# Performance work log

Hardware: AMD Instinct MI355X
Metric: run time of the kernel (lower is better)

Reference implementation:

```python
import jax, jax.numpy as jnp
import numpy as np

HIDDEN = 32
FEATURES = 16
LABELS = 4
T = 8
N = 40000
E = 640000
D_IN = FEATURES + LABELS + HIDDEN + 1  # GATv2Conv input dim = 53


def setup_inputs() -> dict:
    key = jax.random.key(0)
    ks = jax.random.split(key, 16)
    x = jax.random.normal(ks[0], (T, N, FEATURES), dtype=jnp.float32)
    mask = (jax.random.uniform(ks[1], (N,)) < 0.7).astype(jnp.float32)
    labels = jax.random.normal(ks[2], (N, LABELS), dtype=jnp.float32)
    edge_index = jax.random.randint(ks[3], (2, E), 0, N, dtype=jnp.int32)
    edge_weight = jax.random.uniform(ks[4], (E,), dtype=jnp.float32)
    s = 1.0 / np.sqrt(D_IN)
    # 4 GATv2Conv layers stacked: 0=reset, 1=update, 2=cell, 3=final
    Wl = jax.random.normal(ks[5], (4, HIDDEN, D_IN), dtype=jnp.float32) * s
    bl = jnp.zeros((4, HIDDEN), dtype=jnp.float32)
    Wr = jax.random.normal(ks[6], (4, HIDDEN, D_IN), dtype=jnp.float32) * s
    br = jnp.zeros((4, HIDDEN), dtype=jnp.float32)
    att = jax.random.normal(ks[7], (4, HIDDEN), dtype=jnp.float32) * (1.0 / np.sqrt(HIDDEN))
    bconv = jnp.zeros((4, HIDDEN), dtype=jnp.float32)
    W1 = jax.random.normal(ks[8], (FEATURES, HIDDEN), dtype=jnp.float32) * (1.0 / np.sqrt(HIDDEN))
    b1 = jnp.zeros((FEATURES,), dtype=jnp.float32)
    W2 = jax.random.normal(ks[9], (FEATURES, 2 * HIDDEN), dtype=jnp.float32) * (1.0 / np.sqrt(2 * HIDDEN))
    b2 = jnp.zeros((FEATURES,), dtype=jnp.float32)
    return {"x": x, "mask": mask, "labels": labels, "edge_index": edge_index,
            "edge_weight": edge_weight, "Wl": Wl, "bl": bl, "Wr": Wr, "br": br,
            "att": att, "bconv": bconv, "W1": W1, "b1": b1, "W2": W2, "b2": b2}


def gatv2(xin, src, dst, Wl, bl, Wr, br, att, bconv):
    # GATv2Conv, heads=1, add_self_loops=False (edge_weight unused: lin_edge is None)
    xl = xin @ Wl.T + bl          # [N, H] source transform (message)
    xr = xin @ Wr.T + br          # [N, H] target transform
    z = jax.nn.leaky_relu(xl[src] + xr[dst], 0.2)  # [E, H]
    e = z @ att                   # [E] attention logits
    m = jax.ops.segment_max(e, dst, num_segments=N)
    a = jnp.exp(e - m[dst])
    den = jax.ops.segment_sum(a, dst, num_segments=N)[dst]
    a = a / jnp.where(den > 0, den, 1.0)
    out = jax.ops.segment_sum(a[:, None] * xl[src], dst, num_segments=N)
    return out + bconv


def reference(x, mask, labels, edge_index, edge_weight, Wl, bl, Wr, br, att, bconv, W1, b1, W2, b2):
    src, dst = edge_index[0], edge_index[1]
    mcol = mask[:, None]                       # [N, 1] float, concatenated as a feature
    mbool = mcol > 0.5                         # [N, 1] bool, used for where()
    masked_input = jnp.where(mbool[None], x, 0.0)  # [T, N, F]
    hidden0 = jnp.ones((N, HIDDEN), dtype=x.dtype)
    x2_0 = masked_input[0]

    def step(carry, xt):
        hidden, x2 = carry
        ft = jnp.concatenate([x2, mcol, labels], axis=1)        # [N, F+1+L]
        inp = jnp.concatenate([ft, hidden], axis=1)             # [N, D_IN]
        reset = jax.nn.sigmoid(gatv2(inp, src, dst, Wl[0], bl[0], Wr[0], br[0], att[0], bconv[0]))
        update = jax.nn.sigmoid(gatv2(inp, src, dst, Wl[1], bl[1], Wr[1], br[1], att[1], bconv[1]))
        cin = jnp.concatenate([ft, reset * hidden], axis=1)
        cell = jnp.tanh(gatv2(cin, src, dst, Wl[2], bl[2], Wr[2], br[2], att[2], bconv[2]))
        hidden = update * hidden + (1.0 - update) * cell        # (dropout inactive: eval mode)
        y1 = hidden @ W1.T + b1
        x1 = jnp.where(mbool, xt, y1)
        ft2 = jnp.concatenate([x1, mcol, hidden, labels], axis=1)  # [N, D_IN]
        s = jax.nn.relu(gatv2(ft2, src, dst, Wl[3], bl[3], Wr[3], br[3], att[3], bconv[3]))
        y2 = jnp.concatenate([s, hidden], axis=1) @ W2.T + b2
        x2_new = jnp.where(mbool, xt, y2)
        return (hidden, x2_new), x2_new

    _, out = jax.lax.scan(step, (hidden0, x2_0), masked_input)
    return out  # [T, N, F]
```

## Files before the change

### kernel.cpp

```cpp
#include <hip/hip_runtime.h>
#include <math.h>

#define NN   40000
#define EE   640000
#define HID  32
#define FEAT 16
#define LAB  4
#define TT   8
#define DIN  53
#define WD   (HID * DIN)


__device__ __forceinline__ unsigned short f2bf(float f) {
    unsigned int u = __float_as_uint(f);
    unsigned int r = u + 0x7fffu + ((u >> 16) & 1u);
    return (unsigned short)(r >> 16);
}
__device__ __forceinline__ float bflo(unsigned int u) { return __uint_as_float(u << 16); }
__device__ __forceinline__ float bfhi(unsigned int u) { return __uint_as_float(u & 0xffff0000u); }
__device__ __forceinline__ void unpack8(uint4 u, float* v) {
    v[0] = bflo(u.x); v[1] = bfhi(u.x);
    v[2] = bflo(u.y); v[3] = bfhi(u.y);
    v[4] = bflo(u.z); v[5] = bfhi(u.z);
    v[6] = bflo(u.w); v[7] = bfhi(u.w);
}


__global__ __launch_bounds__(256) void zero_i32(int* __restrict__ p, int n) {
    int i = blockIdx.x * 256 + threadIdx.x;
    if (i < n) p[i] = 0;
}

__global__ __launch_bounds__(256) void hist_kernel(const int* __restrict__ dst,
                                                   int* __restrict__ deg) {
    int e = blockIdx.x * 256 + threadIdx.x;
    if (e < EE) atomicAdd(&deg[dst[e]], 1);
}

__global__ __launch_bounds__(1024) void scan_kernel(const int* __restrict__ deg,
                                                    int* __restrict__ row_ptr) {
    __shared__ int wsum[16];
    __shared__ int chunk_total;
    int tid = threadIdx.x;
    int lane = tid & 63, wv = tid >> 6;
    int carry = 0;
    if (tid == 0) row_ptr[0] = 0;
    for (int base = 0; base < NN; base += 1024) {
        int i = base + tid;
        int v = (i < NN) ? deg[i] : 0;
        #pragma unroll
        for (int o = 1; o < 64; o <<= 1) {
            int t = __shfl_up(v, o);
            if (lane >= o) v += t;
        }
        if (lane == 63) wsum[wv] = v;
        __syncthreads();
        if (tid < 16) {
            int s = wsum[tid];
            #pragma unroll
            for (int o = 1; o < 16; o <<= 1) {
                int t = __shfl_up(s, o);
                if (tid >= o) s += t;
            }
            wsum[tid] = s;
            if (tid == 15) chunk_total = s;
        }
        __syncthreads();
        int woff = (wv == 0) ? 0 : wsum[wv - 1];
        if (i < NN) row_ptr[i + 1] = carry + woff + v;
        carry += chunk_total;
        __syncthreads();
    }
}

__global__ __launch_bounds__(256) void scatter_kernel(const int* __restrict__ src,
                                                      const int* __restrict__ dst,
                                                      const int* __restrict__ row_ptr,
                                                      int* __restrict__ cursor,
                                                      int* __restrict__ csr_src) {
    int e = blockIdx.x * 256 + threadIdx.x;
    if (e < EE) {
        int d = dst[e];
        int pos = atomicAdd(&cursor[d], 1);
        csr_src[row_ptr[d] + pos] = src[e];
    }
}

__global__ __launch_bounds__(256) void sort_kernel(const int* __restrict__ row_ptr,
                                                   int* __restrict__ csr_src) {
    int n = blockIdx.x * 256 + threadIdx.x;
    if (n < NN) {
        int beg = row_ptr[n], end = row_ptr[n + 1];
        for (int i = beg + 1; i < end; ++i) {
            int key = csr_src[i];
            int j = i - 1;
            while (j >= beg && csr_src[j] > key) {
                csr_src[j + 1] = csr_src[j];
                --j;
            }
            csr_src[j + 1] = key;
        }
    }
}


__global__ __launch_bounds__(256) void init_kernel(const float* __restrict__ x0,
                                                   const float* __restrict__ mask,
                                                   float* __restrict__ hidden,
                                                   float* __restrict__ x2) {
    int i = blockIdx.x * 256 + threadIdx.x;
    if (i < NN * HID) hidden[i] = 1.0f;
    if (i < NN * FEAT) {
        int node = i >> 4;
        x2[i] = (mask[node] > 0.5f) ? x0[i] : 0.0f;
    }
}


__global__ __launch_bounds__(256) void dense01_kernel(const float* __restrict__ feat,
                                                      const float* __restrict__ mask,
                                                      const float* __restrict__ labels,
                                                      const float* __restrict__ hsrc,
                                                      const float* __restrict__ Wl,
                                                      const float* __restrict__ bl,
                                                      const float* __restrict__ Wr,
                                                      const float* __restrict__ br,
                                                      unsigned short* __restrict__ xl01h,
                                                      float* __restrict__ xr01) {
    __shared__ float W_s[4 * WD];
    __shared__ float inp_s[8][DIN];
    for (int idx = threadIdx.x; idx < WD; idx += 256) {
        W_s[idx]          = Wl[idx];
        W_s[WD + idx]     = Wl[WD + idx];
        W_s[2 * WD + idx] = Wr[idx];
        W_s[3 * WD + idx] = Wr[WD + idx];
    }
    int ni = threadIdx.x >> 5, k = threadIdx.x & 31;
    const float* w0 = &W_s[k * DIN];
    const float* w1 = &W_s[WD + k * DIN];
    const float* w2 = &W_s[2 * WD + k * DIN];
    const float* w3 = &W_s[3 * WD + k * DIN];
    float bl0 = bl[k], bl1 = bl[HID + k], br0 = br[k], br1 = br[HID + k];
#pragma unroll
    for (int it = 0; it < 4; ++it) {
        int node = blockIdx.x * 32 + it * 8 + ni;
        __syncthreads();
        for (int i = k; i < DIN; i += 32) {
            float v;
            if (i < 16)       v = feat[node * 16 + i];
            else if (i == 16) v = mask[node];
            else if (i < 21)  v = labels[node * 4 + (i - 17)];
            else              v = hsrc[node * 32 + (i - 21)];
            inp_s[ni][i] = v;
        }
        __syncthreads();
        float l0 = bl0, l1 = bl1, r0 = br0, r1 = br1;
#pragma unroll
        for (int i = 0; i < DIN; ++i) {
            float xv = inp_s[ni][i];
            l0 += xv * w0[i];
            l1 += xv * w1[i];
            r0 += xv * w2[i];
            r1 += xv * w3[i];
        }
        xl01h[node * 64 + k]      = f2bf(l0);
        xl01h[node * 64 + 32 + k] = f2bf(l1);
        xr01[node * 64 + k]      = r0;
        xr01[node * 64 + 32 + k] = r1;
    }
}


__global__ __launch_bounds__(256) void dense_kernel(const float* __restrict__ feat,
                                                    const float* __restrict__ mask,
                                                    const float* __restrict__ labels,
                                                    const float* __restrict__ hsrc,
                                                    const float* __restrict__ hmul,
                                                    const float* __restrict__ Wl,
                                                    const float* __restrict__ bl,
                                                    const float* __restrict__ Wr,
                                                    const float* __restrict__ br,
                                                    unsigned short* __restrict__ xlh,
                                                    float* __restrict__ xr) {
    __shared__ float Wl_s[WD];
    __shared__ float Wr_s[WD];
    __shared__ float inp_s[8][DIN];
    for (int idx = threadIdx.x; idx < WD; idx += 256) {
        Wl_s[idx] = Wl[idx];
        Wr_s[idx] = Wr[idx];
    }
    int ni = threadIdx.x >> 5, k = threadIdx.x & 31;
    const float* wlr = &Wl_s[k * DIN];
    const float* wrr = &Wr_s[k * DIN];
    float blv = bl[k], brv = br[k];
#pragma unroll
    for (int it = 0; it < 4; ++it) {
        int node = blockIdx.x * 32 + it * 8 + ni;
        __syncthreads();
        for (int i = k; i < DIN; i += 32) {
            float v;
            if (i < 16)       v = feat[node * 16 + i];
            else if (i == 16) v = mask[node];
            else if (i < 21)  v = labels[node * 4 + (i - 17)];
            else              v = hsrc[node * 32 + (i - 21)] * hmul[node * 32 + (i - 21)];
            inp_s[ni][i] = v;
        }
        __syncthreads();
        float al = blv, ar = brv;
#pragma unroll
        for (int i = 0; i < DIN; ++i) {
            float xv = inp_s[ni][i];
            al += xv * wlr[i];
            ar += xv * wrr[i];
        }
        xlh[node * 32 + k] = f2bf(al);
        xr[node * 32 + k] = ar;
    }
}


__device__ __forceinline__ float edge_score8(const float* v, const float* xr, const float* at) {
    float part = 0.0f;
#pragma unroll
    for (int i = 0; i < 8; ++i) {
        float z = v[i] + xr[i];
        z = (z > 0.0f) ? z : 0.2f * z;
        part += z * at[i];
    }
    part += __shfl_xor(part, 1);
    part += __shfl_xor(part, 2);
    return part;
}

__device__ __forceinline__ void online_update8(float e, float& m, float& den, float* acc,
                                               const float* v) {
    if (e > m) {
        float sc = __expf(m - e);
        den *= sc;
#pragma unroll
        for (int i = 0; i < 8; ++i) acc[i] *= sc;
        m = e;
    }
    float a = __expf(e - m);
    den += a;
#pragma unroll
    for (int i = 0; i < 8; ++i) acc[i] += a * v[i];
}

__device__ __forceinline__ void merge_full(float m, float den, const float* acc,
                                           bool ne, float* o) {
    if (ne) {
        float mt = m;
        mt = fmaxf(mt, __shfl_xor(mt, 4));
        mt = fmaxf(mt, __shfl_xor(mt, 8));
        mt = fmaxf(mt, __shfl_xor(mt, 16));
        mt = fmaxf(mt, __shfl_xor(mt, 32));
        float sc = __expf(m - mt);
        float d = den * sc;
        d += __shfl_xor(d, 4);
        d += __shfl_xor(d, 8);
        d += __shfl_xor(d, 16);
        d += __shfl_xor(d, 32);
#pragma unroll
        for (int i = 0; i < 8; ++i) {
            float t = acc[i] * sc;
            t += __shfl_xor(t, 4);
            t += __shfl_xor(t, 8);
            t += __shfl_xor(t, 16);
            t += __shfl_xor(t, 32);
            o[i] = t / d;
        }
    } else {
#pragma unroll
        for (int i = 0; i < 8; ++i) o[i] = 0.0f;
    }
}

__device__ __forceinline__ void merge_half(float m, float den, const float* acc,
                                           bool ne, float* o) {
    if (ne) {
        float mt = m;
        mt = fmaxf(mt, __shfl_xor(mt, 4));
        mt = fmaxf(mt, __shfl_xor(mt, 8));
        mt = fmaxf(mt, __shfl_xor(mt, 16));
        float sc = __expf(m - mt);
        float d = den * sc;
        d += __shfl_xor(d, 4);
        d += __shfl_xor(d, 8);
        d += __shfl_xor(d, 16);
#pragma unroll
        for (int i = 0; i < 8; ++i) {
            float t = acc[i] * sc;
            t += __shfl_xor(t, 4);
            t += __shfl_xor(t, 8);
            t += __shfl_xor(t, 16);
            o[i] = t / d;
        }
    } else {
#pragma unroll
        for (int i = 0; i < 8; ++i) o[i] = 0.0f;
    }
}


__global__ __launch_bounds__(256) void conv01_kernel(const int* __restrict__ row_ptr,
                                                     const int* __restrict__ csr_src,
                                                     const unsigned short* __restrict__ xl01h,
                                                     const float* __restrict__ xr01,
                                                     const float* __restrict__ att,
                                                     const float* __restrict__ bconv,
                                                     float* __restrict__ g0,
                                                     float* __restrict__ g1) {
    int wid  = threadIdx.x >> 6;
    int lane = threadIdx.x & 63;
    int h  = lane >> 5;
    int hl = lane & 31;
    int g = hl >> 2, j = hl & 3;
    int n = blockIdx.x * 4 + wid;
    int c0 = j * 8;
    int beg = row_ptr[n], end = row_ptr[n + 1];

    float at[8], xr[8];
    {
        float4 a0 = *(const float4*)(att + h * 32 + c0);
        float4 a1 = *(const float4*)(att + h * 32 + c0 + 4);
        at[0] = a0.x; at[1] = a0.y; at[2] = a0.z; at[3] = a0.w;
        at[4] = a1.x; at[5] = a1.y; at[6] = a1.z; at[7] = a1.w;
        float4 r0 = *(const float4*)(xr01 + n * 64 + h * 32 + c0);
        float4 r1 = *(const float4*)(xr01 + n * 64 + h * 32 + c0 + 4);
        xr[0] = r0.x; xr[1] = r0.y; xr[2] = r0.z; xr[3] = r0.w;
        xr[4] = r1.x; xr[5] = r1.y; xr[6] = r1.z; xr[7] = r1.w;
    }

    float m = -INFINITY, den = 0.0f, acc[8] = {0, 0, 0, 0, 0, 0, 0, 0};
    for (int p = beg + g; p < end; p += 8) {
        int s = csr_src[p];
        uint4 u = *(const uint4*)(xl01h + (size_t)s * 64 + h * 32 + c0);
        float v[8];
        unpack8(u, v);
        float e = edge_score8(v, xr, at);
        online_update8(e, m, den, acc, v);
    }
    float o[8];
    merge_half(m, den, acc, beg < end, o);

    if (hl < 4) {
        const float* bc = bconv + h * 32 + c0;
        float r[8];
#pragma unroll
        for (int i = 0; i < 8; ++i) r[i] = 1.0f / (1.0f + __expf(-(o[i] + bc[i])));
        float* outp = (h ? g1 : g0) + n * 32 + c0;
        ((float4*)outp)[0] = make_float4(r[0], r[1], r[2], r[3]);
        ((float4*)outp)[1] = make_float4(r[4], r[5], r[6], r[7]);
    }
}


__global__ __launch_bounds__(256) void conv2_kernel(const int* __restrict__ row_ptr,
                                                    const int* __restrict__ csr_src,
                                                    const unsigned short* __restrict__ xlh,
                                                    const float* __restrict__ xr,
                                                    const float* __restrict__ att,
                                                    const float* __restrict__ bconv,
                                                    float* __restrict__ out) {
    int wid  = threadIdx.x >> 6;
    int lane = threadIdx.x & 63;
    int g = lane >> 2, j = lane & 3;
    int n = blockIdx.x * 4 + wid;
    int c0 = j * 8;
    int beg = row_ptr[n], end = row_ptr[n + 1];

    float at[8], xrv[8];
    {
        float4 a0 = *(const float4*)(att + c0);
        float4 a1 = *(const float4*)(att + c0 + 4);
        at[0] = a0.x; at[1] = a0.y; at[2] = a0.z; at[3] = a0.w;
        at[4] = a1.x; at[5] = a1.y; at[6] = a1.z; at[7] = a1.w;
        float4 r0 = *(const float4*)(xr + n * 32 + c0);
        float4 r1 = *(const float4*)(xr + n * 32 + c0 + 4);
        xrv[0] = r0.x; xrv[1] = r0.y; xrv[2] = r0.z; xrv[3] = r0.w;
        xrv[4] = r1.x; xrv[5] = r1.y; xrv[6] = r1.z; xrv[7] = r1.w;
    }

    float m = -INFINITY, den = 0.0f, acc[8] = {0, 0, 0, 0, 0, 0, 0, 0};
    for (int p = beg + g; p < end; p += 16) {
        int s = csr_src[p];
        uint4 u = *(const uint4*)(xlh + (size_t)s * 32 + c0);
        float v[8];
        unpack8(u, v);
        float e = edge_score8(v, xrv, at);
        online_update8(e, m, den, acc, v);
    }
    float o[8];
    merge_full(m, den, acc, beg < end, o);

    if (g == 0) {
        const float* bc = bconv + c0;
        float r[8];
#pragma unroll
        for (int i = 0; i < 8; ++i) r[i] = tanhf(o[i] + bc[i]);
        float* op = out + n * 32 + c0;
        ((float4*)op)[0] = make_float4(r[0], r[1], r[2], r[3]);
        ((float4*)op)[1] = make_float4(r[4], r[5], r[6], r[7]);
    }
}


__global__ __launch_bounds__(256) void conv3_out_kernel(const int* __restrict__ row_ptr,
                                                        const int* __restrict__ csr_src,
                                                        const unsigned short* __restrict__ xlh,
                                                        const float* __restrict__ xr,
                                                        const float* __restrict__ att,
                                                        const float* __restrict__ bconv,
                                                        const float* __restrict__ hidden,
                                                        const float* __restrict__ W2,
                                                        const float* __restrict__ b2,
                                                        const float* __restrict__ x_t,
                                                        const float* __restrict__ mask,
                                                        float* __restrict__ x2,
                                                        float* __restrict__ out_t) {
    __shared__ float W2s[64 * 16];
    for (int idx = threadIdx.x; idx < 64 * 16; idx += 256) {
        int f = idx & 15, c = idx >> 4;
        W2s[c * 16 + f] = W2[f * 64 + c];
    }
    __syncthreads();

    int wid  = threadIdx.x >> 6;
    int lane = threadIdx.x & 63;
    int g = lane >> 2, j = lane & 3;
    int n = blockIdx.x * 4 + wid;
    int c0 = j * 8;
    int beg = row_ptr[n], end = row_ptr[n + 1];

    float at[8], xrv[8];
    {
        float4 a0 = *(const float4*)(att + c0);
        float4 a1 = *(const float4*)(att + c0 + 4);
        at[0] = a0.x; at[1] = a0.y; at[2] = a0.z; at[3] = a0.w;
        at[4] = a1.x; at[5] = a1.y; at[6] = a1.z; at[7] = a1.w;
        float4 r0 = *(const float4*)(xr + n * 32 + c0);
        float4 r1 = *(const float4*)(xr + n * 32 + c0 + 4);
        xrv[0] = r0.x; xrv[1] = r0.y; xrv[2] = r0.z; xrv[3] = r0.w;
        xrv[4] = r1.x; xrv[5] = r1.y; xrv[6] = r1.z; xrv[7] = r1.w;
    }

    float m = -INFINITY, den = 0.0f, acc[8] = {0, 0, 0, 0, 0, 0, 0, 0};
    for (int p = beg + g; p < end; p += 16) {
        int s = csr_src[p];
        uint4 u = *(const uint4*)(xlh + (size_t)s * 32 + c0);
        float v[8];
        unpack8(u, v);
        float e = edge_score8(v, xrv, at);
        online_update8(e, m, den, acc, v);
    }
    float o[8];
    merge_full(m, den, acc, beg < end, o);

    float r[8], hv[8];
    {
        const float* bc = bconv + c0;
#pragma unroll
        for (int i = 0; i < 8; ++i) r[i] = fmaxf(o[i] + bc[i], 0.0f);
        float4 h0 = *(const float4*)(hidden + n * 32 + c0);
        float4 h1 = *(const float4*)(hidden + n * 32 + c0 + 4);
        hv[0] = h0.x; hv[1] = h0.y; hv[2] = h0.z; hv[3] = h0.w;
        hv[4] = h1.x; hv[5] = h1.y; hv[6] = h1.z; hv[7] = h1.w;
    }

    int f = lane & 15;
    int base = lane & ~3;
    float y = b2[f];
#pragma unroll
    for (int j2 = 0; j2 < 4; ++j2) {
#pragma unroll
        for (int i = 0; i < 8; ++i) {
            float sv = __shfl(r[i], base + j2);
            float hh = __shfl(hv[i], base + j2);
            int c = j2 * 8 + i;
            y += sv * W2s[c * 16 + f] + hh * W2s[(32 + c) * 16 + f];
        }
    }
    if (lane < 16) {
        float mv = mask[n];
        float xv = x_t[n * 16 + f];
        float rr = (mv > 0.5f) ? xv : y;
        x2[n * 16 + f] = rr;
        out_t[n * 16 + f] = rr;
    }
}


__global__ __launch_bounds__(256) void update_dense3_kernel(
        const float* __restrict__ g_update, const float* __restrict__ g_cell,
        float* __restrict__ hidden,
        const float* __restrict__ x_t, const float* __restrict__ mask,
        const float* __restrict__ labels,
        const float* __restrict__ W1, const float* __restrict__ b1,
        const float* __restrict__ Wl3, const float* __restrict__ bl3,
        const float* __restrict__ Wr3, const float* __restrict__ br3,
        unsigned short* __restrict__ xlh, float* __restrict__ xr) {
    __shared__ float Wl_s[WD];
    __shared__ float Wr_s[WD];
    __shared__ float W1_s[FEAT * HID];
    __shared__ float inp_s[8][DIN];
    __shared__ float hs[8][HID + 1];
    for (int idx = threadIdx.x; idx < WD; idx += 256) {
        Wl_s[idx] = Wl3[idx];
        Wr_s[idx] = Wr3[idx];
    }
    for (int idx = threadIdx.x; idx < FEAT * HID; idx += 256) W1_s[idx] = W1[idx];
    int ni = threadIdx.x >> 5, k = threadIdx.x & 31;
    const float* wl = &Wl_s[k * DIN];
    const float* wr = &Wr_s[k * DIN];
    float bl3v = bl3[k], br3v = br3[k];
#pragma unroll
    for (int it = 0; it < 4; ++it) {
        int node = blockIdx.x * 32 + it * 8 + ni;
        __syncthreads();
        float u = g_update[node * 32 + k];
        float c = g_cell[node * 32 + k];
        float h = hidden[node * 32 + k];
        float hn = u * h + (1.0f - u) * c;
        hidden[node * 32 + k] = hn;
        hs[ni][k] = hn;
        inp_s[ni][17 + k] = hn;
        if (k == 0) inp_s[ni][16] = mask[node];
        if (k < 4)  inp_s[ni][49 + k] = labels[node * 4 + k];
        __syncthreads();
        if (k < 16) {
            float a = b1[k];
            const float* w = &W1_s[k * 32];
#pragma unroll
            for (int i = 0; i < 32; ++i) a += hs[ni][i] * w[i];
            float mv = mask[node];
            inp_s[ni][k] = (mv > 0.5f) ? x_t[node * 16 + k] : a;
        }
        __syncthreads();
        float al = bl3v, ar = br3v;
#pragma unroll
        for (int i = 0; i < DIN; ++i) {
            float xv = inp_s[ni][i];
            al += xv * wl[i];
            ar += xv * wr[i];
        }
        xlh[node * 32 + k] = f2bf(al);
        xr[node * 32 + k] = ar;
    }
}


extern "C" void kernel_launch(void* const* d_in, const int* in_sizes, int n_in,
                              void* d_out, int out_size, void* d_ws, size_t ws_size,
                              hipStream_t stream) {
    const float* x      = (const float*)d_in[0];
    const float* mask   = (const float*)d_in[1];
    const float* labels = (const float*)d_in[2];
    const int*   src    = (const int*)d_in[3];
    const int*   dst    = src + EE;
    const float* Wl    = (const float*)d_in[5];
    const float* bl    = (const float*)d_in[6];
    const float* Wr    = (const float*)d_in[7];
    const float* br    = (const float*)d_in[8];
    const float* att   = (const float*)d_in[9];
    const float* bconv = (const float*)d_in[10];
    const float* W1    = (const float*)d_in[11];
    const float* b1    = (const float*)d_in[12];
    const float* W2    = (const float*)d_in[13];
    const float* b2    = (const float*)d_in[14];
    float* out = (float*)d_out;

    char* ws = (char*)d_ws;
    size_t off = 0;
    auto alloc = [&](size_t bytes) -> void* {
        void* p = ws + off;
        off = (off + bytes + 255) & ~(size_t)255;
        return p;
    };
    int*   row_ptr = (int*)alloc((NN + 1) * sizeof(int));
    int*   deg     = (int*)alloc(NN * sizeof(int));
    int*   csr_src = (int*)alloc(EE * sizeof(int));
    float* hidden  = (float*)alloc(NN * HID * sizeof(float));
    float* x2      = (float*)alloc(NN * FEAT * sizeof(float));
    unsigned short* xl01h = (unsigned short*)alloc(NN * 64 * sizeof(unsigned short));
    float* xr01    = (float*)alloc(NN * 64 * sizeof(float));
    unsigned short* xlh = (unsigned short*)alloc(NN * 32 * sizeof(unsigned short));
    float* xr      = (float*)alloc(NN * HID * sizeof(float));
    float* g0      = (float*)alloc(NN * HID * sizeof(float));
    float* g1      = (float*)alloc(NN * HID * sizeof(float));
    float* g2      = (float*)alloc(NN * HID * sizeof(float));

    zero_i32<<<(NN + 255) / 256, 256, 0, stream>>>(deg, NN);
    hist_kernel<<<EE / 256, 256, 0, stream>>>(dst, deg);
    scan_kernel<<<1, 1024, 0, stream>>>(deg, row_ptr);
    zero_i32<<<(NN + 255) / 256, 256, 0, stream>>>(deg, NN);
    scatter_kernel<<<EE / 256, 256, 0, stream>>>(src, dst, row_ptr, deg, csr_src);
    sort_kernel<<<(NN + 255) / 256, 256, 0, stream>>>(row_ptr, csr_src);
    init_kernel<<<NN * HID / 256, 256, 0, stream>>>(x, mask, hidden, x2);

    for (int t = 0; t < TT; ++t) {
        const float* xt = x + (size_t)t * NN * FEAT;
        float* out_t = out + (size_t)t * NN * FEAT;
        dense01_kernel<<<NN / 32, 256, 0, stream>>>(x2, mask, labels, hidden,
            Wl, bl, Wr, br, xl01h, xr01);
        conv01_kernel<<<NN / 4, 256, 0, stream>>>(row_ptr, csr_src, xl01h, xr01,
            att, bconv, g0, g1);
        dense_kernel<<<NN / 32, 256, 0, stream>>>(x2, mask, labels, hidden, g0,
            Wl + 2 * WD, bl + 2 * HID, Wr + 2 * WD, br + 2 * HID, xlh, xr);
        conv2_kernel<<<NN / 4, 256, 0, stream>>>(row_ptr, csr_src, xlh, xr,
            att + 2 * HID, bconv + 2 * HID, g2);
        update_dense3_kernel<<<NN / 32, 256, 0, stream>>>(g1, g2, hidden, xt, mask, labels,
            W1, b1, Wl + 3 * WD, bl + 3 * HID, Wr + 3 * WD, br + 3 * HID, xlh, xr);
        conv3_out_kernel<<<NN / 4, 256, 0, stream>>>(row_ptr, csr_src, xlh, xr,
            att + 3 * HID, bconv + 3 * HID, hidden, W2, b2, xt, mask, x2, out_t);
    }
}
```

Measured before the change: 1.926 ms.

## Fuse layer-2/3 dense projections into conv kernels and warp-sort CSR rows

Each per-node dense projection (cell-input projection and update/final-input projection) moves into the epilogue of the preceding attention-aggregation kernel. This drops two kernel launches per timestep and the g0/g2 intermediate round trips through global memory. It also replaces the single-thread insertion sort of CSR neighbor lists with a wavefront bitonic sort for rows of degree at most 64. The cost is that every 4-node block now stages two full weight matrices into shared memory, which means far more redundant weight loads and higher LDS use that may lower occupancy.

```diff
diff --git a/kernel.cpp b/kernel.cpp
--- a/kernel.cpp
+++ b/kernel.cpp
@@ -88,9 +88,27 @@
 
 __global__ __launch_bounds__(256) void sort_kernel(const int* __restrict__ row_ptr,
                                                    int* __restrict__ csr_src) {
-    int n = blockIdx.x * 256 + threadIdx.x;
-    if (n < NN) {
-        int beg = row_ptr[n], end = row_ptr[n + 1];
+    int wid = threadIdx.x >> 6, lane = threadIdx.x & 63;
+    int n = blockIdx.x * 4 + wid;
+    if (n >= NN) return;
+    int beg = row_ptr[n], end = row_ptr[n + 1];
+    int deg = end - beg;
+    if (deg <= 1) return;
+    if (deg <= 64) {
+        int v = (lane < deg) ? csr_src[beg + lane] : 0x7fffffff;
+        #pragma unroll
+        for (int k = 2; k <= 64; k <<= 1) {
+            #pragma unroll
+            for (int jj = k >> 1; jj >= 1; jj >>= 1) {
+                int pv = __shfl_xor(v, jj);
+                bool up = ((lane & k) == 0);
+                bool lower = ((lane & jj) == 0);
+                int mn = min(v, pv), mx = max(v, pv);
+                v = (lower == up) ? mn : mx;
+            }
+        }
+        if (lane < deg) csr_src[beg + lane] = v;
+    } else if (lane == 0) {
         for (int i = beg + 1; i < end; ++i) {
             int key = csr_src[i];
             int j = i - 1;
@@ -171,54 +189,6 @@
 }
 
 
-__global__ __launch_bounds__(256) void dense_kernel(const float* __restrict__ feat,
-                                                    const float* __restrict__ mask,
-                                                    const float* __restrict__ labels,
-                                                    const float* __restrict__ hsrc,
-                                                    const float* __restrict__ hmul,
-                                                    const float* __restrict__ Wl,
-                                                    const float* __restrict__ bl,
-                                                    const float* __restrict__ Wr,
-                                                    const float* __restrict__ br,
-                                                    unsigned short* __restrict__ xlh,
-                                                    float* __restrict__ xr) {
-    __shared__ float Wl_s[WD];
-    __shared__ float Wr_s[WD];
-    __shared__ float inp_s[8][DIN];
-    for (int idx = threadIdx.x; idx < WD; idx += 256) {
-        Wl_s[idx] = Wl[idx];
-        Wr_s[idx] = Wr[idx];
-    }
-    int ni = threadIdx.x >> 5, k = threadIdx.x & 31;
-    const float* wlr = &Wl_s[k * DIN];
-    const float* wrr = &Wr_s[k * DIN];
-    float blv = bl[k], brv = br[k];
-#pragma unroll
-    for (int it = 0; it < 4; ++it) {
-        int node = blockIdx.x * 32 + it * 8 + ni;
-        __syncthreads();
-        for (int i = k; i < DIN; i += 32) {
-            float v;
-            if (i < 16)       v = feat[node * 16 + i];
-            else if (i == 16) v = mask[node];
-            else if (i < 21)  v = labels[node * 4 + (i - 17)];
-            else              v = hsrc[node * 32 + (i - 21)] * hmul[node * 32 + (i - 21)];
-            inp_s[ni][i] = v;
-        }
-        __syncthreads();
-        float al = blv, ar = brv;
-#pragma unroll
-        for (int i = 0; i < DIN; ++i) {
-            float xv = inp_s[ni][i];
-            al += xv * wlr[i];
-            ar += xv * wrr[i];
-        }
-        xlh[node * 32 + k] = f2bf(al);
-        xr[node * 32 + k] = ar;
-    }
-}
-
-
 __device__ __forceinline__ float edge_score8(const float* v, const float* xr, const float* at) {
     float part = 0.0f;
 #pragma unroll
@@ -303,14 +273,25 @@
 }
 
 
-__global__ __launch_bounds__(256) void conv01_kernel(const int* __restrict__ row_ptr,
-                                                     const int* __restrict__ csr_src,
-                                                     const unsigned short* __restrict__ xl01h,
-                                                     const float* __restrict__ xr01,
-                                                     const float* __restrict__ att,
-                                                     const float* __restrict__ bconv,
-                                                     float* __restrict__ g0,
-                                                     float* __restrict__ g1) {
+__global__ __launch_bounds__(256) void conv01_d2_kernel(
+        const int* __restrict__ row_ptr, const int* __restrict__ csr_src,
+        const unsigned short* __restrict__ xl01h, const float* __restrict__ xr01,
+        const float* __restrict__ att, const float* __restrict__ bconv,
+        const float* __restrict__ x2, const float* __restrict__ mask,
+        const float* __restrict__ labels, const float* __restrict__ hidden,
+        const float* __restrict__ Wl2, const float* __restrict__ bl2,
+        const float* __restrict__ Wr2, const float* __restrict__ br2,
+        float* __restrict__ g1,
+        unsigned short* __restrict__ xlh, float* __restrict__ xr) {
+    __shared__ float Wl_s[WD];
+    __shared__ float Wr_s[WD];
+    __shared__ float cin_s[4][DIN + 3];
+    for (int idx = threadIdx.x; idx < WD; idx += 256) {
+        Wl_s[idx] = Wl2[idx];
+        Wr_s[idx] = Wr2[idx];
+    }
+    __syncthreads();
+
     int wid  = threadIdx.x >> 6;
     int lane = threadIdx.x & 63;
     int h  = lane >> 5;
@@ -320,7 +301,7 @@
     int c0 = j * 8;
     int beg = row_ptr[n], end = row_ptr[n + 1];
 
-    float at[8], xr[8];
+    float at[8], xrv[8];
     {
         float4 a0 = *(const float4*)(att + h * 32 + c0);
         float4 a1 = *(const float4*)(att + h * 32 + c0 + 4);
@@ -328,8 +309,8 @@
         at[4] = a1.x; at[5] = a1.y; at[6] = a1.z; at[7] = a1.w;
         float4 r0 = *(const float4*)(xr01 + n * 64 + h * 32 + c0);
         float4 r1 = *(const float4*)(xr01 + n * 64 + h * 32 + c0 + 4);
-        xr[0] = r0.x; xr[1] = r0.y; xr[2] = r0.z; xr[3] = r0.w;
-        xr[4] = r1.x; xr[5] = r1.y; xr[6] = r1.z; xr[7] = r1.w;
+        xrv[0] = r0.x; xrv[1] = r0.y; xrv[2] = r0.z; xrv[3] = r0.w;
+        xrv[4] = r1.x; xrv[5] = r1.y; xrv[6] = r1.z; xrv[7] = r1.w;
     }
 
     float m = -INFINITY, den = 0.0f, acc[8] = {0, 0, 0, 0, 0, 0, 0, 0};
@@ -338,31 +319,70 @@
         uint4 u = *(const uint4*)(xl01h + (size_t)s * 64 + h * 32 + c0);
         float v[8];
         unpack8(u, v);
-        float e = edge_score8(v, xr, at);
+        float e = edge_score8(v, xrv, at);
         online_update8(e, m, den, acc, v);
     }
     float o[8];
     merge_half(m, den, acc, beg < end, o);
 
-    if (hl < 4) {
-        const float* bc = bconv + h * 32 + c0;
-        float r[8];
-#pragma unroll
-        for (int i = 0; i < 8; ++i) r[i] = 1.0f / (1.0f + __expf(-(o[i] + bc[i])));
-        float* outp = (h ? g1 : g0) + n * 32 + c0;
-        ((float4*)outp)[0] = make_float4(r[0], r[1], r[2], r[3]);
-        ((float4*)outp)[1] = make_float4(r[4], r[5], r[6], r[7]);
-    }
-}
-
-
-__global__ __launch_bounds__(256) void conv2_kernel(const int* __restrict__ row_ptr,
-                                                    const int* __restrict__ csr_src,
-                                                    const unsigned short* __restrict__ xlh,
-                                                    const float* __restrict__ xr,
-                                                    const float* __restrict__ att,
-                                                    const float* __restrict__ bconv,
-                                                    float* __restrict__ out) {
+    const float* bc = bconv + h * 32 + c0;
+    float r[8];
+#pragma unroll
+    for (int i = 0; i < 8; ++i) r[i] = 1.0f / (1.0f + __expf(-(o[i] + bc[i])));
+
+    if (h == 1 && g == 0) {
+        float* p1 = g1 + n * 32 + c0;
+        ((float4*)p1)[0] = make_float4(r[0], r[1], r[2], r[3]);
+        ((float4*)p1)[1] = make_float4(r[4], r[5], r[6], r[7]);
+    }
+    if (h == 0 && g == 0) {
+        float4 h0 = *(const float4*)(hidden + n * 32 + c0);
+        float4 h1 = *(const float4*)(hidden + n * 32 + c0 + 4);
+        float hv[8] = {h0.x, h0.y, h0.z, h0.w, h1.x, h1.y, h1.z, h1.w};
+#pragma unroll
+        for (int i = 0; i < 8; ++i) cin_s[wid][21 + c0 + i] = r[i] * hv[i];
+    }
+    if (h == 1 && hl < 21) {
+        int i = hl;
+        float v;
+        if (i < 16)       v = x2[n * 16 + i];
+        else if (i == 16) v = mask[n];
+        else              v = labels[n * 4 + (i - 17)];
+        cin_s[wid][i] = v;
+    }
+    int k = lane & 31;
+    const float* w = (h == 0) ? &Wl_s[k * DIN] : &Wr_s[k * DIN];
+    float a2 = (h == 0) ? bl2[k] : br2[k];
+#pragma unroll
+    for (int i = 0; i < DIN; ++i) a2 += cin_s[wid][i] * w[i];
+    if (h == 0) xlh[n * 32 + k] = f2bf(a2);
+    else        xr[n * 32 + k]  = a2;
+}
+
+
+__global__ __launch_bounds__(256) void conv2_ud3_kernel(
+        const int* __restrict__ row_ptr, const int* __restrict__ csr_src,
+        const unsigned short* __restrict__ xlh, const float* __restrict__ xr,
+        const float* __restrict__ att2, const float* __restrict__ bconv2,
+        const float* __restrict__ g1, float* __restrict__ hidden,
+        const float* __restrict__ x_t, const float* __restrict__ mask,
+        const float* __restrict__ labels,
+        const float* __restrict__ W1, const float* __restrict__ b1,
+        const float* __restrict__ Wl3, const float* __restrict__ bl3,
+        const float* __restrict__ Wr3, const float* __restrict__ br3,
+        unsigned short* __restrict__ xlh2, float* __restrict__ xr2) {
+    __shared__ float Wl_s[WD];
+    __shared__ float Wr_s[WD];
+    __shared__ float W1_s[FEAT * HID];
+    __shared__ float ft2_s[4][DIN + 3];
+    __shared__ float hs[4][HID + 1];
+    for (int idx = threadIdx.x; idx < WD; idx += 256) {
+        Wl_s[idx] = Wl3[idx];
+        Wr_s[idx] = Wr3[idx];
+    }
+    for (int idx = threadIdx.x; idx < FEAT * HID; idx += 256) W1_s[idx] = W1[idx];
+    __syncthreads();
+
     int wid  = threadIdx.x >> 6;
     int lane = threadIdx.x & 63;
     int g = lane >> 2, j = lane & 3;
@@ -372,8 +392,8 @@
 
     float at[8], xrv[8];
     {
-        float4 a0 = *(const float4*)(att + c0);
-        float4 a1 = *(const float4*)(att + c0 + 4);
+        float4 a0 = *(const float4*)(att2 + c0);
+        float4 a1 = *(const float4*)(att2 + c0 + 4);
         at[0] = a0.x; at[1] = a0.y; at[2] = a0.z; at[3] = a0.w;
         at[4] = a1.x; at[5] = a1.y; at[6] = a1.z; at[7] = a1.w;
         float4 r0 = *(const float4*)(xr + n * 32 + c0);
@@ -394,15 +414,49 @@
     float o[8];
     merge_full(m, den, acc, beg < end, o);
 
-    if (g == 0) {
-        const float* bc = bconv + c0;
-        float r[8];
-#pragma unroll
-        for (int i = 0; i < 8; ++i) r[i] = tanhf(o[i] + bc[i]);
-        float* op = out + n * 32 + c0;
-        ((float4*)op)[0] = make_float4(r[0], r[1], r[2], r[3]);
-        ((float4*)op)[1] = make_float4(r[4], r[5], r[6], r[7]);
-    }
+    {
+        const float* bc = bconv2 + c0;
+        float4 h0 = *(const float4*)(hidden + n * 32 + c0);
+        float4 h1 = *(const float4*)(hidden + n * 32 + c0 + 4);
+        float hvv[8] = {h0.x, h0.y, h0.z, h0.w, h1.x, h1.y, h1.z, h1.w};
+        float4 u0 = *(const float4*)(g1 + n * 32 + c0);
+        float4 u1 = *(const float4*)(g1 + n * 32 + c0 + 4);
+        float uv[8] = {u0.x, u0.y, u0.z, u0.w, u1.x, u1.y, u1.z, u1.w};
+        float hn[8];
+#pragma unroll
+        for (int i = 0; i < 8; ++i) {
+            float cell = tanhf(o[i] + bc[i]);
+            hn[i] = uv[i] * hvv[i] + (1.0f - uv[i]) * cell;
+        }
+        if (g == 0) {
+            float* hp = hidden + n * 32 + c0;
+            ((float4*)hp)[0] = make_float4(hn[0], hn[1], hn[2], hn[3]);
+            ((float4*)hp)[1] = make_float4(hn[4], hn[5], hn[6], hn[7]);
+#pragma unroll
+            for (int i = 0; i < 8; ++i) {
+                hs[wid][c0 + i] = hn[i];
+                ft2_s[wid][17 + c0 + i] = hn[i];
+            }
+        }
+    }
+    if (lane == 4) ft2_s[wid][16] = mask[n];
+    if (lane >= 8 && lane < 12) ft2_s[wid][49 + (lane - 8)] = labels[n * 4 + (lane - 8)];
+    if (lane >= 48) {
+        int f = lane - 48;
+        float a = b1[f];
+        const float* w1r = &W1_s[f * 32];
+#pragma unroll
+        for (int c = 0; c < 32; ++c) a += hs[wid][c] * w1r[c];
+        ft2_s[wid][f] = (mask[n] > 0.5f) ? x_t[n * 16 + f] : a;
+    }
+    int k = lane & 31;
+    int h2 = lane >> 5;
+    const float* w = (h2 == 0) ? &Wl_s[k * DIN] : &Wr_s[k * DIN];
+    float a3 = (h2 == 0) ? bl3[k] : br3[k];
+#pragma unroll
+    for (int i = 0; i < DIN; ++i) a3 += ft2_s[wid][i] * w[i];
+    if (h2 == 0) xlh2[n * 32 + k] = f2bf(a3);
+    else         xr2[n * 32 + k]  = a3;
 }
 
 
@@ -487,65 +541,6 @@
         float rr = (mv > 0.5f) ? xv : y;
         x2[n * 16 + f] = rr;
         out_t[n * 16 + f] = rr;
-    }
-}
-
-
-__global__ __launch_bounds__(256) void update_dense3_kernel(
-        const float* __restrict__ g_update, const float* __restrict__ g_cell,
-        float* __restrict__ hidden,
-        const float* __restrict__ x_t, const float* __restrict__ mask,
-        const float* __restrict__ labels,
-        const float* __restrict__ W1, const float* __restrict__ b1,
-        const float* __restrict__ Wl3, const float* __restrict__ bl3,
-        const float* __restrict__ Wr3, const float* __restrict__ br3,
-        unsigned short* __restrict__ xlh, float* __restrict__ xr) {
-    __shared__ float Wl_s[WD];
-    __shared__ float Wr_s[WD];
-    __shared__ float W1_s[FEAT * HID];
-    __shared__ float inp_s[8][DIN];
-    __shared__ float hs[8][HID + 1];
-    for (int idx = threadIdx.x; idx < WD; idx += 256) {
-        Wl_s[idx] = Wl3[idx];
-        Wr_s[idx] = Wr3[idx];
-    }
-    for (int idx = threadIdx.x; idx < FEAT * HID; idx += 256) W1_s[idx] = W1[idx];
-    int ni = threadIdx.x >> 5, k = threadIdx.x & 31;
-    const float* wl = &Wl_s[k * DIN];
-    const float* wr = &Wr_s[k * DIN];
-    float bl3v = bl3[k], br3v = br3[k];
-#pragma unroll
-    for (int it = 0; it < 4; ++it) {
-        int node = blockIdx.x * 32 + it * 8 + ni;
-        __syncthreads();
-        float u = g_update[node * 32 + k];
-        float c = g_cell[node * 32 + k];
-        float h = hidden[node * 32 + k];
-        float hn = u * h + (1.0f - u) * c;
-        hidden[node * 32 + k] = hn;
-        hs[ni][k] = hn;
-        inp_s[ni][17 + k] = hn;
-        if (k == 0) inp_s[ni][16] = mask[node];
-        if (k < 4)  inp_s[ni][49 + k] = labels[node * 4 + k];
-        __syncthreads();
-        if (k < 16) {
-            float a = b1[k];
-            const float* w = &W1_s[k * 32];
-#pragma unroll
-            for (int i = 0; i < 32; ++i) a += hs[ni][i] * w[i];
-            float mv = mask[node];
-            inp_s[ni][k] = (mv > 0.5f) ? x_t[node * 16 + k] : a;
-        }
-        __syncthreads();
-        float al = bl3v, ar = br3v;
-#pragma unroll
-        for (int i = 0; i < DIN; ++i) {
-            float xv = inp_s[ni][i];
-            al += xv * wl[i];
-            ar += xv * wr[i];
-        }
-        xlh[node * 32 + k] = f2bf(al);
-        xr[node * 32 + k] = ar;
     }
 }
 
@@ -584,34 +579,35 @@
     float* x2      = (float*)alloc(NN * FEAT * sizeof(float));
     unsigned short* xl01h = (unsigned short*)alloc(NN * 64 * sizeof(unsigned short));
     float* xr01    = (float*)alloc(NN * 64 * sizeof(float));
-    unsigned short* xlh = (unsigned short*)alloc(NN * 32 * sizeof(unsigned short));
+    unsigned short* xlh  = (unsigned short*)alloc(NN * 32 * sizeof(unsigned short));
     float* xr      = (float*)alloc(NN * HID * sizeof(float));
-    float* g0      = (float*)alloc(NN * HID * sizeof(float));
+    unsigned short* xlh2 = (unsigned short*)alloc(NN * 32 * sizeof(unsigned short));
+    float* xr2     = (float*)alloc(NN * HID * sizeof(float));
     float* g1      = (float*)alloc(NN * HID * sizeof(float));
-    float* g2      = (float*)alloc(NN * HID * sizeof(float));
 
     zero_i32<<<(NN + 255) / 256, 256, 0, stream>>>(deg, NN);
     hist_kernel<<<EE / 256, 256, 0, stream>>>(dst, deg);
     scan_kernel<<<1, 1024, 0, stream>>>(deg, row_ptr);
     zero_i32<<<(NN + 255) / 256, 256, 0, stream>>>(deg, NN);
     scatter_kernel<<<EE / 256, 256, 0, stream>>>(src, dst, row_ptr, deg, csr_src);
-    sort_kernel<<<(NN + 255) / 256, 256, 0, stream>>>(row_ptr, csr_src);
+    sort_kernel<<<NN / 4, 256, 0, stream>>>(row_ptr, csr_src);
     init_kernel<<<NN * HID / 256, 256, 0, stream>>>(x, mask, hidden, x2);
 
+    const int WDc = WD;
     for (int t = 0; t < TT; ++t) {
         const float* xt = x + (size_t)t * NN * FEAT;
         float* out_t = out + (size_t)t * NN * FEAT;
         dense01_kernel<<<NN / 32, 256, 0, stream>>>(x2, mask, labels, hidden,
             Wl, bl, Wr, br, xl01h, xr01);
-        conv01_kernel<<<NN / 4, 256, 0, stream>>>(row_ptr, csr_src, xl01h, xr01,
-            att, bconv, g0, g1);
-        dense_kernel<<<NN / 32, 256, 0, stream>>>(x2, mask, labels, hidden, g0,
-            Wl + 2 * WD, bl + 2 * HID, Wr + 2 * WD, br + 2 * HID, xlh, xr);
-        conv2_kernel<<<NN / 4, 256, 0, stream>>>(row_ptr, csr_src, xlh, xr,
-            att + 2 * HID, bconv + 2 * HID, g2);
-        update_dense3_kernel<<<NN / 32, 256, 0, stream>>>(g1, g2, hidden, xt, mask, labels,
-            W1, b1, Wl + 3 * WD, bl + 3 * HID, Wr + 3 * WD, br + 3 * HID, xlh, xr);
-        conv3_out_kernel<<<NN / 4, 256, 0, stream>>>(row_ptr, csr_src, xlh, xr,
+        conv01_d2_kernel<<<NN / 4, 256, 0, stream>>>(row_ptr, csr_src, xl01h, xr01,
+            att, bconv, x2, mask, labels, hidden,
+            Wl + 2 * WDc, bl + 2 * HID, Wr + 2 * WDc, br + 2 * HID,
+            g1, xlh, xr);
+        conv2_ud3_kernel<<<NN / 4, 256, 0, stream>>>(row_ptr, csr_src, xlh, xr,
+            att + 2 * HID, bconv + 2 * HID, g1, hidden, xt, mask, labels,
+            W1, b1, Wl + 3 * WDc, bl + 3 * HID, Wr + 3 * WDc, br + 3 * HID,
+            xlh2, xr2);
+        conv3_out_kernel<<<NN / 4, 256, 0, stream>>>(row_ptr, csr_src, xlh2, xr2,
             att + 3 * HID, bconv + 3 * HID, hidden, W2, b2, xt, mask, x2, out_t);
     }
 }
```

Result: no change. 1.904 ms (-1.1%).
